# Kernel optimization log

Measured on AMD Instinct MI355X. Metric: run time of the kernel, lower is better.

The kernel has to match this reference:

```python
import jax, jax.numpy as jnp
import numpy as np

B, S, D = 2, 2048, 2048
N_HEADS, N_KV_HEADS = 16, 4
HEAD_DIM = D // N_HEADS


def setup_inputs() -> dict:
    key = jax.random.key(0)
    ks = jax.random.split(key, 5)
    x = jax.random.normal(ks[0], (B, S, D), dtype=jnp.float32)
    W_q = jax.random.normal(ks[1], (D, D), dtype=jnp.float32) * 0.02
    W_k = jax.random.normal(ks[2], (D, N_KV_HEADS * HEAD_DIM), dtype=jnp.float32) * 0.02
    W_v = jax.random.normal(ks[3], (D, N_KV_HEADS * HEAD_DIM), dtype=jnp.float32) * 0.02
    W_o = jax.random.normal(ks[4], (D, D), dtype=jnp.float32) * 0.02
    return {"x": x, "W_q": W_q, "W_k": W_k, "W_v": W_v, "W_o": W_o}


def _apply_rope(xh, positions):
    # xh: [B, H, S, Dh]; rotate adjacent pairs as complex numbers
    Dh = xh.shape[-1]
    half = Dh // 2
    freqs = 1.0 / (10000.0 ** (jnp.arange(half, dtype=jnp.float32) / half))  # [half]
    angles = positions[:, None].astype(jnp.float32) * freqs[None, :]          # [S, half]
    cos, sin = jnp.cos(angles), jnp.sin(angles)
    xp = xh.reshape(*xh.shape[:-1], half, 2)
    x0, x1 = xp[..., 0], xp[..., 1]
    r0 = x0 * cos - x1 * sin
    r1 = x0 * sin + x1 * cos
    return jnp.stack([r0, r1], axis=-1).reshape(xh.shape)


def reference(x, W_q, W_k, W_v, W_o):
    b, s, d = x.shape
    positions = jnp.arange(s)
    rep = N_HEADS // N_KV_HEADS
    Q = (x @ W_q).reshape(b, s, N_HEADS, HEAD_DIM).transpose(0, 2, 1, 3)        # [B,H,S,Dh]
    K = (x @ W_k).reshape(b, s, N_KV_HEADS, HEAD_DIM).transpose(0, 2, 1, 3)     # [B,Hkv,S,Dh]
    V = (x @ W_v).reshape(b, s, N_KV_HEADS, HEAD_DIM).transpose(0, 2, 1, 3)
    Qr = _apply_rope(Q, positions)
    # torch .repeat(1, rep, 1, 1) tiles kv-head blocks: head h -> kv head h % n_kv_heads
    K_rep = jnp.tile(K, (1, rep, 1, 1))
    V_rep = jnp.tile(V, (1, rep, 1, 1))
    Kr = _apply_rope(K_rep, positions)
    scores = jnp.einsum('bhqd,bhkd->bhqk', Qr, Kr) / (HEAD_DIM ** 0.5)
    weights = jax.nn.softmax(scores, axis=-1)
    out = jnp.einsum('bhqk,bhkd->bhqd', weights, V_rep)
    out = out.transpose(0, 2, 1, 3).reshape(b, s, d)
    return out @ W_o
```

## Files before the change

kernel.cpp:

```cpp
#include <hip/hip_runtime.h>


typedef __attribute__((ext_vector_type(8))) short  short8;
typedef __attribute__((ext_vector_type(8))) __bf16 bf16x8;
typedef __attribute__((ext_vector_type(4))) float  f32x4;

#define B_   2
#define S_   2048
#define D_   2048
#define H_   16
#define HKV_ 4
#define DH_  128
#define M_   4096
#define NQKV 3072

static __device__ __forceinline__ ushort f2bf(float f) {
  __bf16 h = (__bf16)f;
  return __builtin_bit_cast(unsigned short, h);
}
static __device__ __forceinline__ float bf2f(ushort u) {
  union { unsigned u; float f; } v; v.u = ((unsigned)u) << 16;
  return v.f;
}
static __device__ __forceinline__ f32x4 mfma16(short8 a, short8 b, f32x4 c) {
  return __builtin_amdgcn_mfma_f32_16x16x32_bf16(
      __builtin_bit_cast(bf16x8, a), __builtin_bit_cast(bf16x8, b), c, 0, 0, 0);
}
static __device__ __forceinline__ void gload16(const ushort* g, ushort* l) {
  __builtin_amdgcn_global_load_lds(
      (const __attribute__((address_space(1))) unsigned int*)g,
      (__attribute__((address_space(3))) unsigned int*)l, 16, 0, 0);
}
template <int N>
static __device__ __forceinline__ void vmwait() {
  asm volatile("s_waitcnt vmcnt(%0)" :: "n"(N) : "memory");
}

__global__ void conv_f32_bf16(const float* __restrict__ in,
                              ushort* __restrict__ out, int n4) {
  int i = blockIdx.x * blockDim.x + threadIdx.x;
  if (i >= n4) return;
  float4 v = ((const float4*)in)[i];
  ushort4 o;
  o.x = f2bf(v.x); o.y = f2bf(v.y); o.z = f2bf(v.z); o.w = f2bf(v.w);
  ((ushort4*)out)[i] = o;
}

__global__ void transpose_conv(const float* __restrict__ in,
                               ushort* __restrict__ out, int R, int C) {
  __shared__ float tile[32][33];
  int c0 = blockIdx.x * 32, r0 = blockIdx.y * 32;
  int tx = threadIdx.x, ty = threadIdx.y;
#pragma unroll
  for (int i = 0; i < 32; i += 8)
    tile[ty + i][tx] = in[(size_t)(r0 + ty + i) * C + c0 + tx];
  __syncthreads();
#pragma unroll
  for (int i = 0; i < 32; i += 8)
    out[(size_t)(c0 + ty + i) * R + r0 + tx] = f2bf(tile[tx][ty + i]);
}

__global__ void transpose_v(const ushort* __restrict__ in,
                            ushort* __restrict__ out, int src_stride) {
  __shared__ ushort tile[32][33];
  int bkv = blockIdx.z;
  const ushort* src = in + (size_t)(bkv >> 2) * S_ * src_stride + (bkv & 3) * DH_;
  ushort* dst = out + (size_t)bkv * DH_ * S_;
  int d0 = blockIdx.x * 32, s0 = blockIdx.y * 32;
  int tx = threadIdx.x, ty = threadIdx.y;
#pragma unroll
  for (int i = 0; i < 32; i += 8)
    tile[ty + i][tx] = src[(size_t)(s0 + ty + i) * src_stride + d0 + tx];
  __syncthreads();
#pragma unroll
  for (int i = 0; i < 32; i += 8)
    dst[(size_t)(d0 + ty + i) * S_ + s0 + tx] = tile[tx][ty + i];
}

__global__ void rope_table_k(float2* __restrict__ tab) {
  int i = blockIdx.x * blockDim.x + threadIdx.x;
  int pos = i >> 6, f = i & 63;
  float freq = powf(10000.0f, -(float)f / 64.0f);
  float a = (float)pos * freq;
  tab[i] = make_float2(cosf(a), sinf(a));
}

__global__ void rope_apply_k(ushort* __restrict__ t,
                             const float2* __restrict__ tab,
                             int total, int ppr_shift, int row_stride,
                             float oscale) {
  int idx = blockIdx.x * blockDim.x + threadIdx.x;
  if (idx >= total) return;
  int row = idx >> ppr_shift;
  int p   = idx & ((1 << ppr_shift) - 1);
  int head = p >> 6, fi = p & 63;
  int pos = row & (S_ - 1);
  float2 cs = tab[(pos << 6) + fi];
  size_t off = (size_t)row * row_stride + head * DH_ + 2 * fi;
  ushort2 v = *(ushort2*)&t[off];
  float x0 = bf2f(v.x), x1 = bf2f(v.y);
  ushort2 o;
  o.x = f2bf((x0 * cs.x - x1 * cs.y) * oscale);
  o.y = f2bf((x0 * cs.y + x1 * cs.x) * oscale);
  *(ushort2*)&t[off] = o;
}

template <int BN, int NF, typename OutT>
__global__ __launch_bounds__(512, 1) void gemm8p(const ushort* __restrict__ A,
                                                 const ushort* __restrict__ Bt,
                                                 OutT* __restrict__ C,
                                                 int M, int N, int K) {
  __shared__ ushort As[2][256 * 64];
  __shared__ ushort Bs[2][BN * 64];
  const int tid = threadIdx.x;
  const int lane = tid & 63, w = tid >> 6;
  const int l16 = lane & 15, l4 = lane >> 4;
  const int wm = (w >> 2) * 128, wn = (w & 3) * (BN / 4);
  const int bm = blockIdx.x * 256, bn = blockIdx.y * BN;
  const int swz = l16 & 7;

  const ushort* gA = A  + (size_t)bm * K;
  const ushort* gB = Bt + (size_t)bn * K;
  const int srow = tid >> 3;
  const int scb  = tid & 7;
  const int sswz = srow & 7;

  auto stageA = [&](int t, int s, int g) {
    int row = g * 64 + srow;
    gload16(gA + (size_t)row * K + t * 64 + ((scb ^ sswz) * 8),
            &As[s][(g * 64 + w * 8) * 64]);
  };
  auto stageB = [&](int t, int s, int g) {
    int row = g * 64 + srow;
    gload16(gB + (size_t)row * K + t * 64 + ((scb ^ sswz) * 8),
            &Bs[s][(g * 64 + w * 8) * 64]);
  };
  auto stageB2 = [&](int t, int s) {
    if constexpr (NF == 3) stageB(t, s, 2);
  };

  constexpr int VM_A = (NF == 3) ? 9 : 8;
  constexpr int VM_B = (NF == 3) ? 7 : 6;

  f32x4 acc[8][NF] = {};
  short8 bfr[NF][2];
  const int NT  = K / 64;
  const int NIT = K / 128;

  stageB(0, 0, 0); stageB(0, 0, 1); stageB2(0, 0);
  stageA(0, 0, 0); stageA(0, 0, 2);
  stageA(0, 0, 1); stageA(0, 0, 3);
  stageB(1, 1, 0); stageB(1, 1, 1); stageB2(1, 1);
  stageA(1, 1, 0); stageA(1, 1, 2);
  vmwait<VM_B>();
  __builtin_amdgcn_s_barrier();
  __builtin_amdgcn_sched_barrier(0);

#define GPHASE(S, J, ISSUES, VMW)                                             \
  {                                                                           \
    short8 afr[2][2];                                                         \
    _Pragma("unroll")                                                         \
    for (int mf = 0; mf < 2; ++mf) {                                          \
      _Pragma("unroll")                                                       \
      for (int kk = 0; kk < 2; ++kk) {                                        \
        int row = wm + (J) * 32 + mf * 16 + l16;                              \
        afr[mf][kk] =                                                         \
            *(const short8*)&As[S][row * 64 + (((kk * 4 + l4) ^ swz) * 8)];   \
      }                                                                       \
    }                                                                         \
    if ((J) == 0) {                                                           \
      _Pragma("unroll")                                                       \
      for (int nf = 0; nf < NF; ++nf) {                                       \
        _Pragma("unroll")                                                     \
        for (int kk = 0; kk < 2; ++kk) {                                      \
          int row = wn + nf * 16 + l16;                                       \
          bfr[nf][kk] =                                                       \
              *(const short8*)&Bs[S][row * 64 + (((kk * 4 + l4) ^ swz) * 8)]; \
        }                                                                     \
      }                                                                       \
    }                                                                         \
    ISSUES;                                                                   \
    __builtin_amdgcn_s_barrier();                                             \
    asm volatile("s_waitcnt lgkmcnt(0)" ::: "memory");                        \
    __builtin_amdgcn_sched_barrier(0);                                        \
    __builtin_amdgcn_s_setprio(1);                                            \
    _Pragma("unroll")                                                         \
    for (int kk = 0; kk < 2; ++kk) {                                          \
      _Pragma("unroll")                                                       \
      for (int mf = 0; mf < 2; ++mf) {                                        \
        _Pragma("unroll")                                                     \
        for (int nf = 0; nf < NF; ++nf)                                       \
          acc[(J) * 2 + mf][nf] =                                             \
              mfma16(afr[mf][kk], bfr[nf][kk], acc[(J) * 2 + mf][nf]);        \
      }                                                                       \
    }                                                                         \
    __builtin_amdgcn_s_setprio(0);                                            \
    VMW;                                                                      \
    __builtin_amdgcn_s_barrier();                                             \
    __builtin_amdgcn_sched_barrier(0);                                        \
  }

  for (int i = 0; i < NIT; ++i) {
    const int tb  = 2 * i + 1;
    const int ta2 = (2 * i + 2 < NT) ? 2 * i + 2 : NT - 1;
    const int tb2 = (2 * i + 3 < NT) ? 2 * i + 3 : NT - 1;
    GPHASE(0, 0, (stageA(tb, 1, 1), stageA(tb, 1, 3)), (void)0)
    GPHASE(0, 1, (stageB(ta2, 0, 0), stageB(ta2, 0, 1)), vmwait<VM_A>())
    GPHASE(0, 2, (stageB2(ta2, 0), stageA(ta2, 0, 0)), (void)0)
    GPHASE(0, 3, (stageA(ta2, 0, 2)), vmwait<VM_B>())
    GPHASE(1, 0, (stageA(ta2, 0, 1), stageA(ta2, 0, 3)), (void)0)
    GPHASE(1, 1, (stageB(tb2, 1, 0), stageB(tb2, 1, 1)), vmwait<VM_A>())
    GPHASE(1, 2, (stageB2(tb2, 1), stageA(tb2, 1, 0)), (void)0)
    GPHASE(1, 3, (stageA(tb2, 1, 2)), vmwait<VM_B>())
  }
#undef GPHASE

  asm volatile("s_waitcnt vmcnt(0)" ::: "memory");

#pragma unroll
  for (int mi = 0; mi < 8; ++mi) {
#pragma unroll
    for (int nf = 0; nf < NF; ++nf) {
#pragma unroll
      for (int r = 0; r < 4; ++r) {
        size_t row = bm + wm + (mi >> 1) * 32 + (mi & 1) * 16 + l4 * 4 + r;
        size_t col = bn + wn + nf * 16 + l16;
        if constexpr (sizeof(OutT) == 2)
          C[row * N + col] = f2bf(acc[mi][nf][r]);
        else
          C[row * N + col] = acc[mi][nf][r];
      }
    }
  }
}

__global__ __launch_bounds__(256, 2) void flash_attn(const ushort* __restrict__ Qp,
                                                     const ushort* __restrict__ Kp,
                                                     const ushort* __restrict__ Vt,
                                                     ushort* __restrict__ Oa) {
  __shared__ ushort Ks[2][64 * 128];
  __shared__ ushort Vs[2][128 * 64];
  const int tid = threadIdx.x;
  const int lane = tid & 63, wave = tid >> 6;
  const int l16 = lane & 15, l4 = lane >> 4;
  const int bh = blockIdx.y;
  const int b = bh >> 4, h = bh & 15, kv = h & 3;
  const int q0 = blockIdx.x * 128 + wave * 32;

  short8 qf[2][4];
#pragma unroll
  for (int qg = 0; qg < 2; ++qg) {
    const ushort* qrow =
        Qp + ((size_t)(b * S_ + q0 + qg * 16 + l16)) * NQKV + h * DH_ + l4 * 8;
#pragma unroll
    for (int kk = 0; kk < 4; ++kk) qf[qg][kk] = *(const short8*)(qrow + kk * 32);
  }

  const ushort* kbase = Kp + (size_t)(b * S_) * NQKV + kv * DH_;
  const ushort* vbase = Vt + (size_t)(b * HKV_ + kv) * DH_ * S_;

  float mreg[2] = {-1e30f, -1e30f};
  f32x4 o[2][8] = {};
  f32x4 ol[2] = {};
  short8 onesf;
#pragma unroll
  for (int j = 0; j < 8; ++j) onesf[j] = (short)0x3F80;

  const int kswz = (l16 & 3) | (((l16 >> 2) & 1) << 2);
  const int vswz = l16 & 7;

  const int krT = wave * 16 + (lane >> 4);
  const int kcT = lane & 15;
  const int vrT = wave * 32 + (lane >> 3);
  const int vcT = lane & 7;

  auto stage = [&](int t, int buf) {
#pragma unroll
    for (int i = 0; i < 4; ++i) {
      int r = krT + i * 4;
      int swzk = (r & 3) | (((r >> 3) & 1) << 2);
      gload16(kbase + (size_t)(t * 64 + r) * NQKV + ((kcT ^ swzk) * 8),
              &Ks[buf][(wave * 16 + i * 4) * 128]);
      int d = vrT + i * 8;
      gload16(vbase + (size_t)d * S_ + t * 64 + ((vcT ^ (d & 7)) * 8),
              &Vs[buf][(wave * 32 + i * 8) * 64]);
    }
  };

  const int NT = S_ / 64;
  stage(0, 0);
  __syncthreads();

  for (int t = 0; t < NT; ++t) {
    const int cur = t & 1;
    if (t + 1 < NT) stage(t + 1, cur ^ 1);

    f32x4 s[2][4] = {};
    __builtin_amdgcn_s_setprio(1);
#pragma unroll
    for (int c = 0; c < 4; ++c) {
      const int krow = 32 * (c >> 1) + 8 * (l16 >> 2) + 4 * (c & 1) + (l16 & 3);
#pragma unroll
      for (int kk = 0; kk < 4; ++kk) {
        short8 kf = *(const short8*)&Ks[cur][krow * 128 + (((kk * 4 + l4) ^ kswz) * 8)];
        s[0][c] = mfma16(kf, qf[0][kk], s[0][c]);
        s[1][c] = mfma16(kf, qf[1][kk], s[1][c]);
      }
    }
    __builtin_amdgcn_s_setprio(0);

    float lmax[2];
#pragma unroll
    for (int qg = 0; qg < 2; ++qg) {
      float a = fmaxf(fmaxf(s[qg][0][0], s[qg][0][1]), fmaxf(s[qg][0][2], s[qg][0][3]));
#pragma unroll
      for (int c = 1; c < 4; ++c) {
        a = fmaxf(a, fmaxf(fmaxf(s[qg][c][0], s[qg][c][1]),
                           fmaxf(s[qg][c][2], s[qg][c][3])));
      }
      lmax[qg] = a;
    }

    bool ok = (lmax[0] - mreg[0] <= 8.0f) && (lmax[1] - mreg[1] <= 8.0f);
    if (!__all(ok)) {
#pragma unroll
      for (int qg = 0; qg < 2; ++qg) {
        float a = fmaxf(lmax[qg], __shfl_xor(lmax[qg], 16));
        float tmax = fmaxf(a, __shfl_xor(a, 32));
        float mn = fmaxf(mreg[qg], tmax);
        float alpha = __builtin_amdgcn_exp2f(mreg[qg] - mn);
        mreg[qg] = mn;
        float af[4];
#pragma unroll
        for (int r = 0; r < 4; ++r)
          af[r] = __shfl(alpha, (lane & 48) + l4 * 4 + r);
#pragma unroll
        for (int g = 0; g < 8; ++g)
#pragma unroll
          for (int r = 0; r < 4; ++r) o[qg][g][r] *= af[r];
#pragma unroll
        for (int r = 0; r < 4; ++r) ol[qg][r] *= af[r];
      }
    }

    short8 pa[2];
#pragma unroll
    for (int ks = 0; ks < 2; ++ks) {
#pragma unroll
      for (int qg = 0; qg < 2; ++qg) {
        short8 pk;
#pragma unroll
        for (int j = 0; j < 8; ++j) {
          float p = __builtin_amdgcn_exp2f(s[qg][2 * ks + (j >> 2)][j & 3] - mreg[qg]);
          pk[j] = (short)f2bf(p);
        }
        pa[qg] = pk;
      }
      __builtin_amdgcn_s_setprio(1);
#pragma unroll
      for (int g = 0; g < 8; ++g) {
        const int d = g * 16 + l16;
        short8 vf = *(const short8*)&Vs[cur][d * 64 + (((ks * 4 + l4) ^ vswz) * 8)];
        o[0][g] = mfma16(pa[0], vf, o[0][g]);
        o[1][g] = mfma16(pa[1], vf, o[1][g]);
      }
      ol[0] = mfma16(pa[0], onesf, ol[0]);
      ol[1] = mfma16(pa[1], onesf, ol[1]);
      __builtin_amdgcn_s_setprio(0);
    }

    __syncthreads();
  }

#pragma unroll
  for (int qg = 0; qg < 2; ++qg) {
    float invq[4];
#pragma unroll
    for (int r = 0; r < 4; ++r) invq[r] = 1.0f / ol[qg][r];
    ushort* op = Oa + (size_t)(b * S_ + q0 + qg * 16) * D_ + h * DH_;
#pragma unroll
    for (int g = 0; g < 8; ++g)
#pragma unroll
      for (int r = 0; r < 4; ++r)
        op[(size_t)(l4 * 4 + r) * D_ + g * 16 + l16] = f2bf(o[qg][g][r] * invq[r]);
  }
}

extern "C" void kernel_launch(void* const* d_in, const int* in_sizes, int n_in,
                              void* d_out, int out_size, void* d_ws, size_t ws_size,
                              hipStream_t stream) {
  (void)in_sizes; (void)n_in; (void)out_size; (void)ws_size;
  const float* x  = (const float*)d_in[0];
  const float* Wq = (const float*)d_in[1];
  const float* Wk = (const float*)d_in[2];
  const float* Wv = (const float*)d_in[3];
  const float* Wo = (const float*)d_in[4];
  float* out = (float*)d_out;

  size_t off = 0;
  auto carve = [&](size_t bytes) -> void* {
    void* p = (char*)d_ws + off;
    off += (bytes + 255) & ~(size_t)255;
    return p;
  };
  ushort* xb    = (ushort*)carve((size_t)M_ * D_ * 2);
  ushort* Wqkvt = (ushort*)carve((size_t)NQKV * D_ * 2);
  ushort* Wot   = (ushort*)carve((size_t)D_ * D_ * 2);
  ushort* QKV   = (ushort*)carve((size_t)M_ * NQKV * 2);
  ushort* Vt    = (ushort*)carve((size_t)M_ * 512 * 2);
  ushort* attn  = (ushort*)carve((size_t)M_ * D_ * 2);
  float2* tab   = (float2*)carve((size_t)S_ * 64 * sizeof(float2));

  conv_f32_bf16<<<(M_ * D_ / 4 + 255) / 256, 256, 0, stream>>>(x, xb, M_ * D_ / 4);
  transpose_conv<<<dim3(64, 64), dim3(32, 8), 0, stream>>>(Wq, Wqkvt, 2048, 2048);
  transpose_conv<<<dim3(16, 64), dim3(32, 8), 0, stream>>>(Wk, Wqkvt + (size_t)2048 * 2048, 2048, 512);
  transpose_conv<<<dim3(16, 64), dim3(32, 8), 0, stream>>>(Wv, Wqkvt + (size_t)2560 * 2048, 2048, 512);
  transpose_conv<<<dim3(64, 64), dim3(32, 8), 0, stream>>>(Wo, Wot, 2048, 2048);
  rope_table_k<<<(S_ * 64) / 256, 256, 0, stream>>>(tab);

  gemm8p<192, 3, ushort><<<dim3(16, 16), 512, 0, stream>>>(xb, Wqkvt, QKV, M_, NQKV, 2048);

  const float qscale = 0.08838834764831845f * 1.4426950408889634f;
  rope_apply_k<<<(M_ * 1024) / 256, 256, 0, stream>>>(QKV, tab, M_ * 1024, 10, NQKV, qscale);
  rope_apply_k<<<(M_ * 256) / 256, 256, 0, stream>>>(QKV + 2048, tab, M_ * 256, 8, NQKV, 1.0f);
  transpose_v<<<dim3(4, 64, 8), dim3(32, 8), 0, stream>>>(QKV + 2560, Vt, NQKV);

  flash_attn<<<dim3(S_ / 128, B_ * H_), 256, 0, stream>>>(QKV, QKV + 2048, Vt, attn);

  gemm8p<128, 2, float><<<dim3(16, 16), 512, 0, stream>>>(attn, Wot, out, M_, 2048, 2048);
}
```

Measured before the change: 216.6 us.

## Fuse prep kernels and rope passes; restructure GEMM to 4-phase 4x2 wave layout

Merges the input conversion, the four weight transpose-converts and the RoPE table build into one launch. The two RoPE passes become a single kernel. Both GEMMs switch from an 8-phase, 2x4-wave schedule to a 4-phase, 4x2-wave schedule with coarser staging per phase, which changes the per-wave fragment shape and the wait counts. This aims to cut launch overhead and simplify the GEMM pipeline, but it risks less overlap between loads and MFMA work and higher register pressure from the larger NF.

```diff
diff --git a/kernel.cpp b/kernel.cpp
--- a/kernel.cpp
+++ b/kernel.cpp
@@ -36,28 +36,48 @@
   asm volatile("s_waitcnt vmcnt(%0)" :: "n"(N) : "memory");
 }
 
-__global__ void conv_f32_bf16(const float* __restrict__ in,
-                              ushort* __restrict__ out, int n4) {
-  int i = blockIdx.x * blockDim.x + threadIdx.x;
-  if (i >= n4) return;
-  float4 v = ((const float4*)in)[i];
-  ushort4 o;
-  o.x = f2bf(v.x); o.y = f2bf(v.y); o.z = f2bf(v.z); o.w = f2bf(v.w);
-  ((ushort4*)out)[i] = o;
-}
-
-__global__ void transpose_conv(const float* __restrict__ in,
-                               ushort* __restrict__ out, int R, int C) {
+__global__ __launch_bounds__(256) void prep(const float* __restrict__ x,
+                                            const float* __restrict__ Wq,
+                                            const float* __restrict__ Wk,
+                                            const float* __restrict__ Wv,
+                                            const float* __restrict__ Wo,
+                                            ushort* __restrict__ xb,
+                                            ushort* __restrict__ Wqkvt,
+                                            ushort* __restrict__ Wot,
+                                            float2* __restrict__ tab) {
   __shared__ float tile[32][33];
-  int c0 = blockIdx.x * 32, r0 = blockIdx.y * 32;
-  int tx = threadIdx.x, ty = threadIdx.y;
+  const int b = blockIdx.x, tid = threadIdx.x;
+  if (b < 8192) {
+    int i = b * 256 + tid;
+    float4 v = ((const float4*)x)[i];
+    ushort4 o;
+    o.x = f2bf(v.x); o.y = f2bf(v.y); o.z = f2bf(v.z); o.w = f2bf(v.w);
+    ((ushort4*)xb)[i] = o;
+    return;
+  }
+  if (b < 8704) {
+    int i = (b - 8704 + 512) * 256 + tid;
+    int pos = i >> 6, f = i & 63;
+    float freq = powf(10000.0f, -(float)f / 64.0f);
+    float a = (float)pos * freq;
+    tab[i] = make_float2(cosf(a), sinf(a));
+    return;
+  }
+  int t = b - 8704;
+  const float* src; ushort* dst; int R, C, bx, by;
+  if (t < 4096)      { src = Wq; dst = Wqkvt;                        R = 2048; C = 2048; bx = t & 63; by = t >> 6; }
+  else if (t < 5120) { t -= 4096; src = Wk; dst = Wqkvt + (size_t)2048 * 2048; R = 2048; C = 512;  bx = t & 15; by = t >> 4; }
+  else if (t < 6144) { t -= 5120; src = Wv; dst = Wqkvt + (size_t)2560 * 2048; R = 2048; C = 512;  bx = t & 15; by = t >> 4; }
+  else               { t -= 6144; src = Wo; dst = Wot;                R = 2048; C = 2048; bx = t & 63; by = t >> 6; }
+  int c0 = bx * 32, r0 = by * 32;
+  int tx = tid & 31, ty = tid >> 5;
 #pragma unroll
   for (int i = 0; i < 32; i += 8)
-    tile[ty + i][tx] = in[(size_t)(r0 + ty + i) * C + c0 + tx];
+    tile[ty + i][tx] = src[(size_t)(r0 + ty + i) * C + c0 + tx];
   __syncthreads();
 #pragma unroll
   for (int i = 0; i < 32; i += 8)
-    out[(size_t)(c0 + ty + i) * R + r0 + tx] = f2bf(tile[tx][ty + i]);
+    dst[(size_t)(c0 + ty + i) * R + r0 + tx] = f2bf(tile[tx][ty + i]);
 }
 
 __global__ void transpose_v(const ushort* __restrict__ in,
@@ -77,26 +97,19 @@
     dst[(size_t)(d0 + ty + i) * S_ + s0 + tx] = tile[tx][ty + i];
 }
 
-__global__ void rope_table_k(float2* __restrict__ tab) {
-  int i = blockIdx.x * blockDim.x + threadIdx.x;
-  int pos = i >> 6, f = i & 63;
-  float freq = powf(10000.0f, -(float)f / 64.0f);
-  float a = (float)pos * freq;
-  tab[i] = make_float2(cosf(a), sinf(a));
-}
-
-__global__ void rope_apply_k(ushort* __restrict__ t,
-                             const float2* __restrict__ tab,
-                             int total, int ppr_shift, int row_stride,
-                             float oscale) {
+__global__ void rope_both(ushort* __restrict__ qkv,
+                          const float2* __restrict__ tab, float qscale) {
   int idx = blockIdx.x * blockDim.x + threadIdx.x;
-  if (idx >= total) return;
+  const int total_q = M_ * 1024;
+  ushort* t; int ppr_shift; float oscale;
+  if (idx < total_q) { t = qkv; ppr_shift = 10; oscale = qscale; }
+  else { idx -= total_q; t = qkv + 2048; ppr_shift = 8; oscale = 1.0f; }
   int row = idx >> ppr_shift;
   int p   = idx & ((1 << ppr_shift) - 1);
   int head = p >> 6, fi = p & 63;
   int pos = row & (S_ - 1);
   float2 cs = tab[(pos << 6) + fi];
-  size_t off = (size_t)row * row_stride + head * DH_ + 2 * fi;
+  size_t off = (size_t)row * NQKV + head * DH_ + 2 * fi;
   ushort2 v = *(ushort2*)&t[off];
   float x0 = bf2f(v.x), x1 = bf2f(v.y);
   ushort2 o;
@@ -106,16 +119,17 @@
 }
 
 template <int BN, int NF, typename OutT>
-__global__ __launch_bounds__(512, 1) void gemm8p(const ushort* __restrict__ A,
+__global__ __launch_bounds__(512, 1) void gemm4p(const ushort* __restrict__ A,
                                                  const ushort* __restrict__ Bt,
                                                  OutT* __restrict__ C,
                                                  int M, int N, int K) {
   __shared__ ushort As[2][256 * 64];
   __shared__ ushort Bs[2][BN * 64];
+  constexpr int NBR = BN / 64;
   const int tid = threadIdx.x;
   const int lane = tid & 63, w = tid >> 6;
   const int l16 = lane & 15, l4 = lane >> 4;
-  const int wm = (w >> 2) * 128, wn = (w & 3) * (BN / 4);
+  const int wm = (w >> 1) * 64, wn = (w & 1) * (BN / 2);
   const int bm = blockIdx.x * 256, bn = blockIdx.y * BN;
   const int swz = l16 & 7;
 
@@ -130,29 +144,28 @@
     gload16(gA + (size_t)row * K + t * 64 + ((scb ^ sswz) * 8),
             &As[s][(g * 64 + w * 8) * 64]);
   };
-  auto stageB = [&](int t, int s, int g) {
-    int row = g * 64 + srow;
-    gload16(gB + (size_t)row * K + t * 64 + ((scb ^ sswz) * 8),
-            &Bs[s][(g * 64 + w * 8) * 64]);
+  auto stageA4 = [&](int t, int s) {
+#pragma unroll
+    for (int g = 0; g < 4; ++g) stageA(t, s, g);
   };
-  auto stageB2 = [&](int t, int s) {
-    if constexpr (NF == 3) stageB(t, s, 2);
+  auto stageBall = [&](int t, int s) {
+#pragma unroll
+    for (int g = 0; g < NBR; ++g) {
+      int row = g * 64 + srow;
+      gload16(gB + (size_t)row * K + t * 64 + ((scb ^ sswz) * 8),
+              &Bs[s][(g * 64 + w * 8) * 64]);
+    }
   };
 
-  constexpr int VM_A = (NF == 3) ? 9 : 8;
-  constexpr int VM_B = (NF == 3) ? 7 : 6;
-
-  f32x4 acc[8][NF] = {};
+  f32x4 acc[4][NF] = {};
   short8 bfr[NF][2];
   const int NT  = K / 64;
   const int NIT = K / 128;
 
-  stageB(0, 0, 0); stageB(0, 0, 1); stageB2(0, 0);
-  stageA(0, 0, 0); stageA(0, 0, 2);
-  stageA(0, 0, 1); stageA(0, 0, 3);
-  stageB(1, 1, 0); stageB(1, 1, 1); stageB2(1, 1);
-  stageA(1, 1, 0); stageA(1, 1, 2);
-  vmwait<VM_B>();
+  stageBall(0, 0);
+  stageA4(0, 0);
+  stageBall(1, 1);
+  vmwait<NBR>();
   __builtin_amdgcn_s_barrier();
   __builtin_amdgcn_sched_barrier(0);
 
@@ -201,24 +214,20 @@
   }
 
   for (int i = 0; i < NIT; ++i) {
-    const int tb  = 2 * i + 1;
-    const int ta2 = (2 * i + 2 < NT) ? 2 * i + 2 : NT - 1;
-    const int tb2 = (2 * i + 3 < NT) ? 2 * i + 3 : NT - 1;
-    GPHASE(0, 0, (stageA(tb, 1, 1), stageA(tb, 1, 3)), (void)0)
-    GPHASE(0, 1, (stageB(ta2, 0, 0), stageB(ta2, 0, 1)), vmwait<VM_A>())
-    GPHASE(0, 2, (stageB2(ta2, 0), stageA(ta2, 0, 0)), (void)0)
-    GPHASE(0, 3, (stageA(ta2, 0, 2)), vmwait<VM_B>())
-    GPHASE(1, 0, (stageA(ta2, 0, 1), stageA(ta2, 0, 3)), (void)0)
-    GPHASE(1, 1, (stageB(tb2, 1, 0), stageB(tb2, 1, 1)), vmwait<VM_A>())
-    GPHASE(1, 2, (stageB2(tb2, 1), stageA(tb2, 1, 0)), (void)0)
-    GPHASE(1, 3, (stageA(tb2, 1, 2)), vmwait<VM_B>())
+    const int tb = 2 * i + 1;
+    const int t2 = (2 * i + 2 < NT) ? 2 * i + 2 : NT - 1;
+    const int t3 = (2 * i + 3 < NT) ? 2 * i + 3 : NT - 1;
+    GPHASE(0, 0, (stageA4(tb, 1)),  (void)0)
+    GPHASE(0, 1, (stageBall(t2, 0)), vmwait<NBR>())
+    GPHASE(1, 0, (stageA4(t2, 0)),  (void)0)
+    GPHASE(1, 1, (stageBall(t3, 1)), vmwait<NBR>())
   }
 #undef GPHASE
 
   asm volatile("s_waitcnt vmcnt(0)" ::: "memory");
 
 #pragma unroll
-  for (int mi = 0; mi < 8; ++mi) {
+  for (int mi = 0; mi < 4; ++mi) {
 #pragma unroll
     for (int nf = 0; nf < NF; ++nf) {
 #pragma unroll
@@ -411,21 +420,15 @@
   ushort* attn  = (ushort*)carve((size_t)M_ * D_ * 2);
   float2* tab   = (float2*)carve((size_t)S_ * 64 * sizeof(float2));
 
-  conv_f32_bf16<<<(M_ * D_ / 4 + 255) / 256, 256, 0, stream>>>(x, xb, M_ * D_ / 4);
-  transpose_conv<<<dim3(64, 64), dim3(32, 8), 0, stream>>>(Wq, Wqkvt, 2048, 2048);
-  transpose_conv<<<dim3(16, 64), dim3(32, 8), 0, stream>>>(Wk, Wqkvt + (size_t)2048 * 2048, 2048, 512);
-  transpose_conv<<<dim3(16, 64), dim3(32, 8), 0, stream>>>(Wv, Wqkvt + (size_t)2560 * 2048, 2048, 512);
-  transpose_conv<<<dim3(64, 64), dim3(32, 8), 0, stream>>>(Wo, Wot, 2048, 2048);
-  rope_table_k<<<(S_ * 64) / 256, 256, 0, stream>>>(tab);
-
-  gemm8p<192, 3, ushort><<<dim3(16, 16), 512, 0, stream>>>(xb, Wqkvt, QKV, M_, NQKV, 2048);
+  prep<<<18944, 256, 0, stream>>>(x, Wq, Wk, Wv, Wo, xb, Wqkvt, Wot, tab);
+
+  gemm4p<192, 6, ushort><<<dim3(16, 16), 512, 0, stream>>>(xb, Wqkvt, QKV, M_, NQKV, 2048);
 
   const float qscale = 0.08838834764831845f * 1.4426950408889634f;
-  rope_apply_k<<<(M_ * 1024) / 256, 256, 0, stream>>>(QKV, tab, M_ * 1024, 10, NQKV, qscale);
-  rope_apply_k<<<(M_ * 256) / 256, 256, 0, stream>>>(QKV + 2048, tab, M_ * 256, 8, NQKV, 1.0f);
+  rope_both<<<(M_ * 1280) / 256, 256, 0, stream>>>(QKV, tab, qscale);
   transpose_v<<<dim3(4, 64, 8), dim3(32, 8), 0, stream>>>(QKV + 2560, Vt, NQKV);
 
   flash_attn<<<dim3(S_ / 128, B_ * H_), 256, 0, stream>>>(QKV, QKV + 2048, Vt, attn);
 
-  gemm8p<128, 2, float><<<dim3(16, 16), 512, 0, stream>>>(attn, Wot, out, M_, 2048, 2048);
-}
+  gemm4p<128, 4, float><<<dim3(16, 16), 512, 0, stream>>>(attn, Wot, out, M_, 2048, 2048);
+}
```

New measurement: 198.5 us. -8.4%, faster.
